# Performance work log

Hardware: AMD Instinct MI355X
Metric: run time of the kernel (lower is better)

Reference implementation:

```python
import jax, jax.numpy as jnp
import numpy as np

B, T, C = 2, 192, 512
H, D = 8, 64  # num_heads, head_dim; inner_dim = H*D = C


def setup_inputs() -> dict:
    key = jax.random.key(0)
    k1, k2, k3 = jax.random.split(key, 3)
    x = jax.random.normal(k1, (B, T, C), dtype=jnp.float32)
    W_in = jax.random.normal(k2, (C, 5 * H * D), dtype=jnp.float32) * 0.02
    b_in = jnp.zeros((5 * H * D,), dtype=jnp.float32)
    W_out = jax.random.normal(k3, (H * D, C), dtype=jnp.float32) * 0.02
    b_out = jnp.zeros((C,), dtype=jnp.float32)
    return {"x": x, "W_in": W_in, "b_in": b_in, "W_out": W_out, "b_out": b_out}


def _split_heads(t):
    # (B,T,H*D) -> (B,H,T,D)
    return t.reshape(B, T, H, D).transpose(0, 2, 1, 3)


def reference(x, W_in, b_in, W_out, b_out):
    scale = D ** -0.5
    proj = x @ W_in + b_in  # (B,T,5*H*D)
    q, k1, v1, k2, v2 = jnp.split(proj, 5, axis=-1)
    q = _split_heads(q) * scale
    k1 = _split_heads(k1)
    v1 = _split_heads(v1)
    k2 = _split_heads(k2)
    v2 = _split_heads(v2)
    # trilinear logits: <q_i, k1_j, k2_k> / sqrt(D), computed in fp32
    logits = jnp.einsum('bhid,bhjd,bhkd->bhijk', q, k1, k2,
                        preferred_element_type=jnp.float32)
    # softmax over the joint (j,k) axes
    attn = jax.nn.softmax(logits.reshape(B, H, T, T * T), axis=-1)
    attn = attn.reshape(B, H, T, T, T).astype(x.dtype)
    # out_i[d] = sum_{j,k} attn[i,j,k] * v1_j[d] * v2_k[d]
    out = jnp.einsum('bhijk,bhjd,bhkd->bhid', attn, v1, v2)
    y = out.transpose(0, 2, 1, 3).reshape(B, T, H * D)  # merge heads
    return y @ W_out + b_out
```

## Files before the change

### kernel.cpp

```cpp
#include <hip/hip_runtime.h>
#include <hip/hip_bf16.h>


typedef float  v4f __attribute__((ext_vector_type(4)));
typedef short  v8s __attribute__((ext_vector_type(8)));

__device__ __forceinline__ unsigned short f2bf(float f) {
  unsigned u = __float_as_uint(f);
  u += 0x7fffu + ((u >> 16) & 1u);
  return (unsigned short)(u >> 16);
}
__device__ __forceinline__ float bf2f(unsigned short b) {
  return __uint_as_float(((unsigned)b) << 16);
}
__device__ __forceinline__ unsigned pack_bf16(float lo, float hi) {
  __hip_bfloat162 t = __float22bfloat162_rn(float2{lo, hi});
  union { __hip_bfloat162 b; unsigned u; } cv;
  cv.b = t;
  return cv.u;
}

#if __has_builtin(__builtin_amdgcn_exp2f)
#define EXP2F(x) __builtin_amdgcn_exp2f(x)
#else
#define EXP2F(x) exp2f(x)
#endif

#define MFMA32(a, b, c) __builtin_amdgcn_mfma_f32_16x16x32_bf16((a), (b), (c), 0, 0, 0)

#define QSCALE 0.18033688011112042f


#define XH_OFF   589824
#define XL_OFF   786432
#define WTH_OFF  983040
#define WTL_OFF  2293760
#define WOTH_OFF 3604480
#define WOTL_OFF 3866624

__device__ __forceinline__ int v1perm_inv(int p) {
  return (((p >> 3) & 3) << 2) | (((p >> 2) & 1) << 4) | (p & 3);
}

__global__ __launch_bounds__(256) void prep_kernel(
    const float* __restrict__ x, const float* __restrict__ Win,
    const float* __restrict__ Wout, unsigned short* __restrict__ wsh) {
  __shared__ float tile[32 * 65];
  const int bi = blockIdx.x, t = threadIdx.x;
  if (bi < 768) {
    const float* W; unsigned short *Th, *Tl; int R, n0, k0;
    if (bi < 640) {
      W = Win; Th = wsh + WTH_OFF; Tl = wsh + WTL_OFF; R = 2560;
      n0 = (bi % 40) << 6; k0 = (bi / 40) << 5;
    } else {
      const int idx = bi - 640;
      W = Wout; Th = wsh + WOTH_OFF; Tl = wsh + WOTL_OFF; R = 512;
      n0 = (idx & 7) << 6; k0 = (idx >> 3) << 5;
    }
    const int n = t & 63, kq = (t >> 6) * 8;
#pragma unroll
    for (int j = 0; j < 8; ++j)
      tile[(kq + j) * 65 + n] = W[(k0 + kq + j) * R + n0 + n];
    __syncthreads();
    const int n2 = t >> 2, ks = (t & 3) * 8;
    union { uint4 u; unsigned short us[8]; } ph, pl;
#pragma unroll
    for (int j = 0; j < 8; ++j) {
      const float v = tile[(ks + j) * 65 + n2];
      const unsigned short h = f2bf(v);
      ph.us[j] = h;
      pl.us[j] = f2bf(v - bf2f(h));
    }
    *(uint4*)(Th + (n0 + n2) * 512 + k0 + ks) = ph.u;
    *(uint4*)(Tl + (n0 + n2) * 512 + k0 + ks) = pl.u;
  } else {
    const int flat = ((bi - 768) * 256 + t) * 8;
    const v4f v0 = *(const v4f*)(x + flat);
    const v4f v1 = *(const v4f*)(x + flat + 4);
    union { uint4 u; unsigned short us[8]; } ph, pl;
#pragma unroll
    for (int j = 0; j < 4; ++j) {
      unsigned short h = f2bf(v0[j]);
      ph.us[j] = h; pl.us[j] = f2bf(v0[j] - bf2f(h));
      h = f2bf(v1[j]);
      ph.us[4 + j] = h; pl.us[4 + j] = f2bf(v1[j] - bf2f(h));
    }
    *(uint4*)(wsh + XH_OFF + flat) = ph.u;
    *(uint4*)(wsh + XL_OFF + flat) = pl.u;
  }
}

__global__ __launch_bounds__(64) void proj_kernel(
    const unsigned short* __restrict__ wsh, const float* __restrict__ bin,
    float* __restrict__ wsf, unsigned short* __restrict__ wshd) {
  __shared__ float tile[32 * 33];
  const int lane = threadIdx.x;
  const int c = lane & 15, q = lane >> 4;
  const int bm = blockIdx.x % 12, bn = blockIdx.x / 12;

  const unsigned short* base[8];
  base[0] = wsh + XH_OFF + (bm * 32 + c) * 512 + (q << 3);
  base[1] = base[0] + 16 * 512;
  base[2] = wsh + XL_OFF + (bm * 32 + c) * 512 + (q << 3);
  base[3] = base[2] + 16 * 512;
  base[4] = wsh + WTH_OFF + (bn * 32 + c) * 512 + (q << 3);
  base[5] = base[4] + 16 * 512;
  base[6] = wsh + WTL_OFF + (bn * 32 + c) * 512 + (q << 3);
  base[7] = base[6] + 16 * 512;

  const v4f z = {0.f, 0.f, 0.f, 0.f};
  v4f a00 = z, a01 = z, a10 = z, a11 = z;

  v8s cur[8], nxt[8];
#pragma unroll
  for (int i = 0; i < 8; ++i) cur[i] = *(const v8s*)(base[i]);
#pragma unroll
  for (int i = 0; i < 8; ++i) nxt[i] = *(const v8s*)(base[i] + 32);

#pragma unroll 1
  for (int ks = 0; ks < 16; ++ks) {
    v8s nx2[8];
    if (ks < 14) {
      const int o = (ks + 2) * 32;
#pragma unroll
      for (int i = 0; i < 8; ++i) nx2[i] = *(const v8s*)(base[i] + o);
    }
    a00 = MFMA32(cur[2], cur[4], a00); a00 = MFMA32(cur[0], cur[6], a00); a00 = MFMA32(cur[0], cur[4], a00);
    a01 = MFMA32(cur[2], cur[5], a01); a01 = MFMA32(cur[0], cur[7], a01); a01 = MFMA32(cur[0], cur[5], a01);
    a10 = MFMA32(cur[3], cur[4], a10); a10 = MFMA32(cur[1], cur[6], a10); a10 = MFMA32(cur[1], cur[4], a10);
    a11 = MFMA32(cur[3], cur[5], a11); a11 = MFMA32(cur[1], cur[7], a11); a11 = MFMA32(cur[1], cur[5], a11);
#pragma unroll
    for (int i = 0; i < 8; ++i) { cur[i] = nxt[i]; nxt[i] = nx2[i]; }
  }

  const int n0 = bn * 32;
  const int which = n0 >> 9;
  const int h  = (n0 & 511) >> 6;
  const int d0 = n0 & 63;
  const int b  = (bm >= 6) ? 1 : 0;
  const int bh = b * 8 + h;
  const int tt0 = (bm - b * 6) * 32;

  v4f accs[2][2] = {{a00, a01}, {a10, a11}};
#pragma unroll
  for (int mt = 0; mt < 2; ++mt)
#pragma unroll
    for (int nt = 0; nt < 2; ++nt) {
      const float bv = bin[n0 + nt * 16 + c];
#pragma unroll
      for (int r = 0; r < 4; ++r)
        tile[(mt * 16 + (q << 2) + r) * 33 + nt * 16 + c] = accs[mt][nt][r] + bv;
    }
  __syncthreads();

  const int rr = lane >> 1, cc0 = (lane & 1) * 16;
  if (which == 0 || which == 4) {
    float* out = wsf + (which == 4 ? 196608 : 0) + ((bh * 192 + tt0 + rr) << 6) + d0 + cc0;
    const float s = (which == 0) ? QSCALE : 1.0f;
#pragma unroll
    for (int i = 0; i < 16; i += 4) {
      v4f v;
#pragma unroll
      for (int j = 0; j < 4; ++j) v[j] = tile[rr * 33 + cc0 + i + j] * s;
      *(v4f*)(out + i) = v;
    }
  } else if (which == 1 || which == 3) {
    unsigned short* out = wshd + (which == 3 ? 196608 : 0) + ((bh * 192 + tt0 + rr) << 6) + d0 + cc0;
#pragma unroll
    for (int hf = 0; hf < 2; ++hf) {
      union { uint4 u; unsigned short us[8]; } pk;
#pragma unroll
      for (int j = 0; j < 8; ++j) pk.us[j] = f2bf(tile[rr * 33 + cc0 + hf * 8 + j]);
      *(uint4*)(out + hf * 8) = pk.u;
    }
  } else {
    const int dd = rr, p0 = cc0;
    unsigned short* out = wshd + 393216 + ((bh << 6) + d0 + dd) * 192 + tt0 + p0;
#pragma unroll
    for (int hf = 0; hf < 2; ++hf) {
      union { uint4 u; unsigned short us[8]; } pk;
#pragma unroll
      for (int j = 0; j < 8; ++j) {
        const int p = p0 + hf * 8 + j;
        pk.us[j] = f2bf(tile[v1perm_inv(p) * 33 + dd]);
      }
      *(uint4*)(out + hf * 8) = pk.u;
    }
  }
}

__global__ __launch_bounds__(256, 3) void attn_kernel(
    const float* __restrict__ wsf, const unsigned short* __restrict__ wsh,
    float* __restrict__ accp, float* __restrict__ Sp) {
  __shared__ char smem[31744];
  unsigned short* V1s = (unsigned short*)smem;
  unsigned short* K2s = (unsigned short*)(smem + 25600);

  const int tid  = threadIdx.x;
  const int wv   = tid >> 6;
  const int lane = tid & 63;
  const int c    = lane & 15;
  const int quad = lane >> 4;
  const int jh   = wv & 1;
  const int kh   = wv >> 1;

  const int bb = blockIdx.x;
  const int kb = bb & 3;
  const int it = (bb >> 2) % 12;
  const int bh = bb / 48;

  const unsigned short* k1g = wsh + bh * 192 * 64;
  const unsigned short* v1g = wsh + 393216 + bh * 64 * 192;
  const unsigned short* k2g = wsh + 196608 + bh * 192 * 64;
  const float*          v2g = wsf + 196608 + bh * 12288;

  for (int idx = tid; idx < 1920; idx += 256) {
    if (idx < 1536) {
      const int r = idx / 24, c8 = (idx % 24) * 8;
      *(uint4*)(V1s + r * 200 + c8) = *(const uint4*)(v1g + r * 192 + c8);
    } else {
      const int j = idx - 1536;
      const int r = j >> 3, c8 = (j & 7) * 8;
      *(uint4*)(K2s + r * 64 + c8) = *(const uint4*)(k2g + (kb * 48 + r) * 64 + c8);
    }
  }

  v8s k1f[6][2];
#pragma unroll
  for (int j = 0; j < 6; ++j) {
    const unsigned short* kp = k1g + (((jh * 6 + j) * 16 + c) << 6) + (quad << 3);
    k1f[j][0] = *(const v8s*)(kp);
    k1f[j][1] = *(const v8s*)(kp + 32);
  }

  const float* qg = wsf + ((bh * 192 + it * 16 + c) << 6) + (quad << 3);
  float q0[8], q1[8];
  {
    v4f qa = *(const v4f*)(qg), qb = *(const v4f*)(qg + 4);
    v4f qc = *(const v4f*)(qg + 32), qd = *(const v4f*)(qg + 36);
#pragma unroll
    for (int e = 0; e < 4; ++e) {
      q0[e] = qa[e]; q0[4 + e] = qb[e];
      q1[e] = qc[e]; q1[4 + e] = qd[e];
    }
  }
  __syncthreads();

  const unsigned short* v1base = V1s + c * 200 + jh * 96 + (quad << 3);

  const v4f z = {0.f, 0.f, 0.f, 0.f};
  v4f acc[4] = {z, z, z, z};
  float sS = 0.f;

  union U4 { uint4 u4; unsigned short us[8]; };
  union AF { v8s v; unsigned u[4]; };

#pragma unroll 1
  for (int ks = 0; ks < 24; ++ks) {
    const int rl = kh * 24 + ks;
    U4 kl, khh;
    kl.u4  = *(const uint4*)(K2s + (rl << 6) + (quad << 3));
    khh.u4 = *(const uint4*)(K2s + (rl << 6) + (quad << 3) + 32);

    AF af0, af1;
#pragma unroll
    for (int e = 0; e < 4; ++e) {
      af0.u[e] = pack_bf16(q0[2*e] * bf2f(kl.us[2*e]),  q0[2*e+1] * bf2f(kl.us[2*e+1]));
      af1.u[e] = pack_bf16(q1[2*e] * bf2f(khh.us[2*e]), q1[2*e+1] * bf2f(khh.us[2*e+1]));
    }

    v4f o0 = z, o1 = z, o2 = z, o3 = z;
#pragma unroll
    for (int m = 0; m < 3; ++m) {
      v4f Ca = MFMA32(k1f[2*m][0],   af0.v, z);
      Ca = MFMA32(k1f[2*m][1],   af1.v, Ca);
      v4f Cb = MFMA32(k1f[2*m+1][0], af0.v, z);
      Cb = MFMA32(k1f[2*m+1][1], af1.v, Cb);
#pragma unroll
      for (int r = 0; r < 4; ++r) { Ca[r] = EXP2F(Ca[r]); Cb[r] = EXP2F(Cb[r]); }
      sS += Ca[0] + Ca[1] + Ca[2] + Ca[3] + Cb[0] + Cb[1] + Cb[2] + Cb[3];
      AF pp;
      pp.u[0] = pack_bf16(Ca[0], Ca[1]);
      pp.u[1] = pack_bf16(Ca[2], Ca[3]);
      pp.u[2] = pack_bf16(Cb[0], Cb[1]);
      pp.u[3] = pack_bf16(Cb[2], Cb[3]);
      const v8s vf0 = *(const v8s*)(v1base + m * 32);
      const v8s vf1 = *(const v8s*)(v1base + 16 * 200 + m * 32);
      const v8s vf2 = *(const v8s*)(v1base + 32 * 200 + m * 32);
      const v8s vf3 = *(const v8s*)(v1base + 48 * 200 + m * 32);
      o0 = MFMA32(vf0, pp.v, o0);
      o1 = MFMA32(vf1, pp.v, o1);
      o2 = MFMA32(vf2, pp.v, o2);
      o3 = MFMA32(vf3, pp.v, o3);
    }
    const float* vb = v2g + ((kb * 48 + rl) << 6) + (quad << 2);
    acc[0] += o0 * (*(const v4f*)(vb));
    acc[1] += o1 * (*(const v4f*)(vb + 16));
    acc[2] += o2 * (*(const v4f*)(vb + 32));
    acc[3] += o3 * (*(const v4f*)(vb + 48));
  }

  __syncthreads();
  float* redA = (float*)smem;
  float* redS = (float*)smem + 4096;

#pragma unroll
  for (int dt = 0; dt < 4; ++dt)
    *(v4f*)(redA + wv * 1024 + (c << 6) + (dt << 4) + (quad << 2)) = acc[dt];
  redS[wv * 64 + (quad << 4) + c] = sS;
  __syncthreads();

  const int pbase = (bh * 12 + it) * 4 + kb;
  float* ap_out = accp + pbase * 1024;
  for (int idx = tid; idx < 1024; idx += 256)
    ap_out[idx] = redA[idx] + redA[1024 + idx] + redA[2048 + idx] + redA[3072 + idx];
  if (tid < 16) {
    float s = 0.f;
#pragma unroll
    for (int w = 0; w < 4; ++w)
#pragma unroll
      for (int qq = 0; qq < 4; ++qq)
        s += redS[w * 64 + qq * 16 + tid];
    Sp[pbase * 16 + tid] = s;
  }
}

__global__ __launch_bounds__(256) void outp2_kernel(
    const float* __restrict__ wsf, const unsigned short* __restrict__ wsh,
    const float* __restrict__ bout, float* __restrict__ y) {
  __shared__ unsigned short OHs[16 * 520];
  __shared__ unsigned short OLs[16 * 520];
  const float* accp = wsf + 393216;
  const float* Sp   = wsf + 1179648;

  const int tid = threadIdx.x;
  const int nq  = blockIdx.x & 3;
  const int bit = blockIdx.x >> 2;
  const int b = bit / 12, it = bit % 12;
  const int m0 = b * 192 + it * 16;

  {
    const int i = tid >> 4, cc0 = (tid & 15) * 32;
    const int h = cc0 >> 6;
    const int pb = ((b * 8 + h) * 12 + it) * 4;
    const float inv = 1.0f / (Sp[pb * 16 + i] + Sp[(pb + 1) * 16 + i] +
                              Sp[(pb + 2) * 16 + i] + Sp[(pb + 3) * 16 + i]);
    const float* ap = accp + pb * 1024 + (i << 6) + (cc0 & 63);
#pragma unroll
    for (int g = 0; g < 8; ++g) {
      v4f a = *(const v4f*)(ap + g * 4);
      a += *(const v4f*)(ap + 1024 + g * 4);
      a += *(const v4f*)(ap + 2048 + g * 4);
      a += *(const v4f*)(ap + 3072 + g * 4);
#pragma unroll
      for (int j = 0; j < 4; ++j) {
        const float v = a[j] * inv;
        const unsigned short hh = f2bf(v);
        OHs[i * 520 + cc0 + g * 4 + j] = hh;
        OLs[i * 520 + cc0 + g * 4 + j] = f2bf(v - bf2f(hh));
      }
    }
  }
  __syncthreads();

  const int lane = tid & 63, wv = tid >> 6;
  const int c = lane & 15, q = lane >> 4;
  const int n0w = nq * 128 + wv * 32;
  const v4f z = {0.f, 0.f, 0.f, 0.f};
  v4f acc[2] = {z, z};

  const unsigned short* Bhb = wsh + WOTH_OFF;
  const unsigned short* Blb = wsh + WOTL_OFF;

  v8s cB[4], nB[4];
#pragma unroll
  for (int nt = 0; nt < 2; ++nt) {
    const int n = n0w + nt * 16 + c;
    cB[nt * 2]     = *(const v8s*)(Bhb + n * 512 + (q << 3));
    cB[nt * 2 + 1] = *(const v8s*)(Blb + n * 512 + (q << 3));
    nB[nt * 2]     = *(const v8s*)(Bhb + n * 512 + 32 + (q << 3));
    nB[nt * 2 + 1] = *(const v8s*)(Blb + n * 512 + 32 + (q << 3));
  }

#pragma unroll 1
  for (int ks = 0; ks < 16; ++ks) {
    v8s x2[4];
    if (ks < 14) {
      const int o = (ks + 2) * 32 + (q << 3);
#pragma unroll
      for (int nt = 0; nt < 2; ++nt) {
        const int n = n0w + nt * 16 + c;
        x2[nt * 2]     = *(const v8s*)(Bhb + n * 512 + o);
        x2[nt * 2 + 1] = *(const v8s*)(Blb + n * 512 + o);
      }
    }
    const v8s Ah = *(const v8s*)(OHs + c * 520 + ks * 32 + (q << 3));
    const v8s Al = *(const v8s*)(OLs + c * 520 + ks * 32 + (q << 3));
#pragma unroll
    for (int nt = 0; nt < 2; ++nt) {
      acc[nt] = MFMA32(Al, cB[nt * 2],     acc[nt]);
      acc[nt] = MFMA32(Ah, cB[nt * 2 + 1], acc[nt]);
      acc[nt] = MFMA32(Ah, cB[nt * 2],     acc[nt]);
    }
#pragma unroll
    for (int i2 = 0; i2 < 4; ++i2) { cB[i2] = nB[i2]; nB[i2] = x2[i2]; }
  }

#pragma unroll
  for (int nt = 0; nt < 2; ++nt) {
    const int n = n0w + nt * 16 + c;
    const float bv = bout[n];
#pragma unroll
    for (int r = 0; r < 4; ++r)
      y[(m0 + (q << 2) + r) * 512 + n] = acc[nt][r] + bv;
  }
}

extern "C" void kernel_launch(void* const* d_in, const int* in_sizes, int n_in,
                              void* d_out, int out_size, void* d_ws, size_t ws_size,
                              hipStream_t stream) {
  const float* x    = (const float*)d_in[0];
  const float* Win  = (const float*)d_in[1];
  const float* bin  = (const float*)d_in[2];
  const float* Wout = (const float*)d_in[3];
  const float* bout = (const float*)d_in[4];

  float* wsf = (float*)d_ws;
  unsigned short* wsh = (unsigned short*)(wsf + 1191936);
  float* accp = wsf + 393216;
  float* Sp   = wsf + 1179648;

  prep_kernel<<<dim3(864), 256, 0, stream>>>(x, Win, Wout, wsh);
  proj_kernel<<<dim3(960), 64, 0, stream>>>(wsh, bin, wsf, wsh);
  attn_kernel<<<dim3(768), 256, 0, stream>>>(wsf, wsh, accp, Sp);
  outp2_kernel<<<dim3(96), 256, 0, stream>>>(wsf, wsh, bout, (float*)d_out);
}
```

Measured before the change: 165.6 us.

## Shrink projection tiles to 16x16 for more blocks and lower attention occupancy hint

The projection GEMM moves from 32x32 output tiles per 64-thread block to 16x16 tiles, quadrupling the grid from 960 to 3840 blocks. The epilogue is rewritten for the smaller tile, including a new index mapping for the permuted V1 transposed store. Separately, the attention kernel's launch bounds change from 3 to 2 minimum blocks per SM, which gives the compiler more registers. More blocks should improve occupancy and latency hiding in the projection, at the cost of less data reuse per block and more redundant loads.

```diff
diff --git a/kernel.cpp b/kernel.cpp
--- a/kernel.cpp
+++ b/kernel.cpp
@@ -93,103 +93,83 @@
 __global__ __launch_bounds__(64) void proj_kernel(
     const unsigned short* __restrict__ wsh, const float* __restrict__ bin,
     float* __restrict__ wsf, unsigned short* __restrict__ wshd) {
-  __shared__ float tile[32 * 33];
+  __shared__ float tile[16 * 17];
   const int lane = threadIdx.x;
   const int c = lane & 15, q = lane >> 4;
-  const int bm = blockIdx.x % 12, bn = blockIdx.x / 12;
-
-  const unsigned short* base[8];
-  base[0] = wsh + XH_OFF + (bm * 32 + c) * 512 + (q << 3);
-  base[1] = base[0] + 16 * 512;
-  base[2] = wsh + XL_OFF + (bm * 32 + c) * 512 + (q << 3);
-  base[3] = base[2] + 16 * 512;
-  base[4] = wsh + WTH_OFF + (bn * 32 + c) * 512 + (q << 3);
-  base[5] = base[4] + 16 * 512;
-  base[6] = wsh + WTL_OFF + (bn * 32 + c) * 512 + (q << 3);
-  base[7] = base[6] + 16 * 512;
+  const int bm = blockIdx.x % 24, bn = blockIdx.x / 24;
+
+  const unsigned short* A0 = wsh + XH_OFF  + (bm * 16 + c) * 512 + (q << 3);
+  const unsigned short* A1 = wsh + XL_OFF  + (bm * 16 + c) * 512 + (q << 3);
+  const unsigned short* B0 = wsh + WTH_OFF + (bn * 16 + c) * 512 + (q << 3);
+  const unsigned short* B1 = wsh + WTL_OFF + (bn * 16 + c) * 512 + (q << 3);
 
   const v4f z = {0.f, 0.f, 0.f, 0.f};
-  v4f a00 = z, a01 = z, a10 = z, a11 = z;
-
-  v8s cur[8], nxt[8];
-#pragma unroll
-  for (int i = 0; i < 8; ++i) cur[i] = *(const v8s*)(base[i]);
-#pragma unroll
-  for (int i = 0; i < 8; ++i) nxt[i] = *(const v8s*)(base[i] + 32);
+  v4f acc = z;
+
+  v8s cA0 = *(const v8s*)(A0),      cA1 = *(const v8s*)(A1);
+  v8s cB0 = *(const v8s*)(B0),      cB1 = *(const v8s*)(B1);
+  v8s nA0 = *(const v8s*)(A0 + 32), nA1 = *(const v8s*)(A1 + 32);
+  v8s nB0 = *(const v8s*)(B0 + 32), nB1 = *(const v8s*)(B1 + 32);
 
 #pragma unroll 1
   for (int ks = 0; ks < 16; ++ks) {
-    v8s nx2[8];
+    v8s xA0, xA1, xB0, xB1;
     if (ks < 14) {
       const int o = (ks + 2) * 32;
-#pragma unroll
-      for (int i = 0; i < 8; ++i) nx2[i] = *(const v8s*)(base[i] + o);
-    }
-    a00 = MFMA32(cur[2], cur[4], a00); a00 = MFMA32(cur[0], cur[6], a00); a00 = MFMA32(cur[0], cur[4], a00);
-    a01 = MFMA32(cur[2], cur[5], a01); a01 = MFMA32(cur[0], cur[7], a01); a01 = MFMA32(cur[0], cur[5], a01);
-    a10 = MFMA32(cur[3], cur[4], a10); a10 = MFMA32(cur[1], cur[6], a10); a10 = MFMA32(cur[1], cur[4], a10);
-    a11 = MFMA32(cur[3], cur[5], a11); a11 = MFMA32(cur[1], cur[7], a11); a11 = MFMA32(cur[1], cur[5], a11);
-#pragma unroll
-    for (int i = 0; i < 8; ++i) { cur[i] = nxt[i]; nxt[i] = nx2[i]; }
-  }
-
-  const int n0 = bn * 32;
+      xA0 = *(const v8s*)(A0 + o); xA1 = *(const v8s*)(A1 + o);
+      xB0 = *(const v8s*)(B0 + o); xB1 = *(const v8s*)(B1 + o);
+    }
+    acc = MFMA32(cA1, cB0, acc);
+    acc = MFMA32(cA0, cB1, acc);
+    acc = MFMA32(cA0, cB0, acc);
+    cA0 = nA0; cA1 = nA1; cB0 = nB0; cB1 = nB1;
+    nA0 = xA0; nA1 = xA1; nB0 = xB0; nB1 = xB1;
+  }
+
+  const int n0 = bn * 16;
   const int which = n0 >> 9;
   const int h  = (n0 & 511) >> 6;
   const int d0 = n0 & 63;
-  const int b  = (bm >= 6) ? 1 : 0;
+  const int b  = (bm >= 12) ? 1 : 0;
   const int bh = b * 8 + h;
-  const int tt0 = (bm - b * 6) * 32;
-
-  v4f accs[2][2] = {{a00, a01}, {a10, a11}};
-#pragma unroll
-  for (int mt = 0; mt < 2; ++mt)
-#pragma unroll
-    for (int nt = 0; nt < 2; ++nt) {
-      const float bv = bin[n0 + nt * 16 + c];
-#pragma unroll
-      for (int r = 0; r < 4; ++r)
-        tile[(mt * 16 + (q << 2) + r) * 33 + nt * 16 + c] = accs[mt][nt][r] + bv;
-    }
+  const int tt0 = (bm - b * 12) * 16;
+
+  const float bv = bin[n0 + c];
+#pragma unroll
+  for (int r = 0; r < 4; ++r)
+    tile[((q << 2) + r) * 17 + c] = acc[r] + bv;
   __syncthreads();
 
-  const int rr = lane >> 1, cc0 = (lane & 1) * 16;
+  const int rr = lane >> 2, g = lane & 3;
   if (which == 0 || which == 4) {
-    float* out = wsf + (which == 4 ? 196608 : 0) + ((bh * 192 + tt0 + rr) << 6) + d0 + cc0;
+    float* out = wsf + (which == 4 ? 196608 : 0) +
+                 ((bh * 192 + tt0 + rr) << 6) + d0 + (g << 2);
     const float s = (which == 0) ? QSCALE : 1.0f;
-#pragma unroll
-    for (int i = 0; i < 16; i += 4) {
-      v4f v;
-#pragma unroll
-      for (int j = 0; j < 4; ++j) v[j] = tile[rr * 33 + cc0 + i + j] * s;
-      *(v4f*)(out + i) = v;
-    }
+    v4f v;
+#pragma unroll
+    for (int j = 0; j < 4; ++j) v[j] = tile[rr * 17 + (g << 2) + j] * s;
+    *(v4f*)out = v;
   } else if (which == 1 || which == 3) {
-    unsigned short* out = wshd + (which == 3 ? 196608 : 0) + ((bh * 192 + tt0 + rr) << 6) + d0 + cc0;
-#pragma unroll
-    for (int hf = 0; hf < 2; ++hf) {
-      union { uint4 u; unsigned short us[8]; } pk;
-#pragma unroll
-      for (int j = 0; j < 8; ++j) pk.us[j] = f2bf(tile[rr * 33 + cc0 + hf * 8 + j]);
-      *(uint4*)(out + hf * 8) = pk.u;
-    }
+    unsigned short* out = wshd + (which == 3 ? 196608 : 0) +
+                          ((bh * 192 + tt0 + rr) << 6) + d0 + (g << 2);
+    union { unsigned long long u; unsigned short us[4]; } pk;
+#pragma unroll
+    for (int j = 0; j < 4; ++j) pk.us[j] = f2bf(tile[rr * 17 + (g << 2) + j]);
+    *(unsigned long long*)out = pk.u;
   } else {
-    const int dd = rr, p0 = cc0;
-    unsigned short* out = wshd + 393216 + ((bh << 6) + d0 + dd) * 192 + tt0 + p0;
-#pragma unroll
-    for (int hf = 0; hf < 2; ++hf) {
-      union { uint4 u; unsigned short us[8]; } pk;
-#pragma unroll
-      for (int j = 0; j < 8; ++j) {
-        const int p = p0 + hf * 8 + j;
-        pk.us[j] = f2bf(tile[v1perm_inv(p) * 33 + dd]);
-      }
-      *(uint4*)(out + hf * 8) = pk.u;
-    }
-  }
-}
-
-__global__ __launch_bounds__(256, 3) void attn_kernel(
+    const int dd = rr;
+    const int hi = (tt0 >> 4) & 1, cb = tt0 & ~31;
+    unsigned short* out = wshd + 393216 + ((bh << 6) + d0 + dd) * 192 +
+                          cb + g * 8 + hi * 4;
+    union { unsigned long long u; unsigned short us[4]; } pk;
+#pragma unroll
+    for (int j = 0; j < 4; ++j)
+      pk.us[j] = f2bf(tile[(g * 4 + j) * 17 + dd]);
+    *(unsigned long long*)out = pk.u;
+  }
+}
+
+__global__ __launch_bounds__(256, 2) void attn_kernel(
     const float* __restrict__ wsf, const unsigned short* __restrict__ wsh,
     float* __restrict__ accp, float* __restrict__ Sp) {
   __shared__ char smem[31744];
@@ -431,7 +411,7 @@
   float* Sp   = wsf + 1179648;
 
   prep_kernel<<<dim3(864), 256, 0, stream>>>(x, Win, Wout, wsh);
-  proj_kernel<<<dim3(960), 64, 0, stream>>>(wsh, bin, wsf, wsh);
+  proj_kernel<<<dim3(3840), 64, 0, stream>>>(wsh, bin, wsf, wsh);
   attn_kernel<<<dim3(768), 256, 0, stream>>>(wsf, wsh, accp, Sp);
   outp2_kernel<<<dim3(96), 256, 0, stream>>>(wsf, wsh, bout, (float*)d_out);
 }
```

After: 158.8 us. -4.1%, faster.
